# Optimization experiments

Hardware: AMD Instinct MI355X
Metric: run time of the kernel (lower is better)

The kernel has to match this reference:

```python
import jax, jax.numpy as jnp
import numpy as np

# FP4 E2M1 magnitude lookup table (3-bit magnitude index)
FP4_LUT = jnp.array([0.0, 0.5, 1.0, 1.5, 2.0, 3.0, 4.0, 6.0], dtype=jnp.float32)
E8M0_BIAS = 127


def setup_inputs() -> dict:
    key = jax.random.key(0)
    k_in, k_pw, k_sc, k_b = jax.random.split(key, 4)
    B, S, I, O, BS = 4, 2048, 4096, 11008, 32
    inp = jax.random.normal(k_in, (B, S, I), dtype=jnp.float32)
    # packed MXFP4 codes: two 4-bit codes per byte
    packed_weight = jax.random.randint(k_pw, (O, I // 2), 0, 256, dtype=jnp.int32)
    # E8M0 exponents near the bias so dequantized magnitudes are O(1)
    weight_scales = jax.random.randint(k_sc, (O, I // BS), 118, 132, dtype=jnp.int32)
    bias = jax.random.normal(k_b, (O,), dtype=jnp.float32) * 0.02
    return {"input": inp, "bias": bias, "packed_weight": packed_weight,
            "weight_scales": weight_scales}


def _dequantize_mxfp4(packed_weight, weight_scales):
    O, P = packed_weight.shape
    I = P * 2
    bs = I // weight_scales.shape[1]
    lo = packed_weight & 0xF          # first element of each pair: low nibble
    hi = (packed_weight >> 4) & 0xF   # second element: high nibble
    codes = jnp.stack([lo, hi], axis=-1).reshape(O, I)  # [O, I]
    mag = FP4_LUT[codes & 0x7]
    sign = jnp.where((codes & 0x8) > 0, -1.0, 1.0)
    vals = sign * mag                                   # [O, I] fp4 values
    scale = jnp.exp2((weight_scales - E8M0_BIAS).astype(jnp.float32))  # [O, I/bs]
    w = (vals.reshape(O, I // bs, bs) * scale[:, :, None]).reshape(O, I)
    return w


def reference(input, bias, packed_weight, weight_scales):
    # quantized-inference path: on-the-fly block dequant + F.linear
    w = _dequantize_mxfp4(packed_weight, weight_scales)  # [O, I]
    out = jnp.einsum('bsi,oi->bso', input, w) + bias     # [B, S, O]
    return out
```

## Files before the change

### kernel.cpp

```cpp
#include <hip/hip_runtime.h>
#include <stdint.h>

typedef __attribute__((ext_vector_type(8))) short bf16x8;
typedef __attribute__((ext_vector_type(8))) unsigned short u16x8;
typedef __attribute__((ext_vector_type(4))) float f32x4;
typedef __attribute__((ext_vector_type(4))) int i32x4;

static constexpr int MDIM = 8192;
static constexpr int KDIM = 4096;
static constexpr int NDIM = 11008;
static constexpr int BM = 256, BN = 256, BK = 32;
static constexpr int NT = KDIM / BK;
static constexpr int NBX = NDIM / BN;
static constexpr int NBY = MDIM / BM;


static __device__ __forceinline__ unsigned short f2bf(float f) {
  unsigned int u = __builtin_bit_cast(unsigned int, f);
  return (unsigned short)((u + 0x7FFFu + ((u >> 16) & 1u)) >> 16);
}

static __device__ __forceinline__ float fp4_val(unsigned int c) {
  unsigned int m = c & 1u, e = (c >> 1) & 3u, s = (c >> 3) & 1u;
  unsigned int bits = e ? (((126u + e) << 23) | (m << 22)) : (m ? 0x3F000000u : 0u);
  bits |= s << 31;
  return __builtin_bit_cast(float, bits);
}

__global__ __launch_bounds__(256) void convert_a_kernel(
    const float4* __restrict__ in, u16x8* __restrict__ out, int n8) {
  int i = blockIdx.x * 256 + threadIdx.x;
  if (i >= n8) return;
  float4 v0 = in[2 * (size_t)i];
  float4 v1 = in[2 * (size_t)i + 1];
  u16x8 r;
  r[0] = f2bf(v0.x); r[1] = f2bf(v0.y); r[2] = f2bf(v0.z); r[3] = f2bf(v0.w);
  r[4] = f2bf(v1.x); r[5] = f2bf(v1.y); r[6] = f2bf(v1.z); r[7] = f2bf(v1.w);
  out[i] = r;
}

__global__ __launch_bounds__(256) void dequant_w_kernel(
    const int* __restrict__ pw, const int* __restrict__ sc,
    unsigned short* __restrict__ wout) {
  int tid = blockIdx.x * 256 + threadIdx.x;
  int o = tid >> 7;
  int b = tid & 127;
  if (o >= NDIM) return;
  const i32x4* src = (const i32x4*)(pw + (size_t)o * (KDIM / 2) + b * 16);
  unsigned int e = (unsigned int)sc[(size_t)o * (KDIM / 32) + b];
  float scale = __builtin_bit_cast(float, e << 23);
  unsigned short* dst = wout + (size_t)o * KDIM + b * 32;
#pragma unroll
  for (int v = 0; v < 4; ++v) {
    i32x4 w4 = src[v];
    u16x8 r;
#pragma unroll
    for (int j = 0; j < 4; ++j) {
      unsigned int w = (unsigned int)w4[j];
      r[2 * j]     = f2bf(fp4_val(w & 0xFu) * scale);
      r[2 * j + 1] = f2bf(fp4_val((w >> 4) & 0xFu) * scale);
    }
    *(u16x8*)(dst + 8 * v) = r;
  }
}


#define GLDS16(gp, lp)                                                                  \
  __builtin_amdgcn_global_load_lds((const __attribute__((address_space(1))) void*)(gp), \
                                   (__attribute__((address_space(3))) void*)(lp), 16, 0, 0)

template <int CS, int NS, bool STAGE, bool LAST>
__device__ __forceinline__ void k_iter(
    unsigned char* lds, int p0, int p1,
    const unsigned short*& gA0, const unsigned short*& gA1,
    const unsigned short*& gB0, const unsigned short*& gB1,
    int baseA, int baseB, f32x4 (&acc)[8][4]) {
  if (LAST) asm volatile("s_waitcnt vmcnt(0)" ::: "memory");
  else      asm volatile("s_waitcnt vmcnt(4)" ::: "memory");
  __builtin_amdgcn_s_barrier();
  asm volatile("" ::: "memory");
  if (STAGE) {
    GLDS16(gA0, lds + NS * 32768 + p0);
    GLDS16(gA1, lds + NS * 32768 + p1);
    GLDS16(gB0, lds + NS * 32768 + 16384 + p0);
    GLDS16(gB1, lds + NS * 32768 + 16384 + p1);
    gA0 += BK; gA1 += BK; gB0 += BK; gB1 += BK;
  }
  const unsigned char* sa = lds + CS * 32768;
  const unsigned char* sb = sa + 16384;
  bf16x8 a[4], b[4];
#pragma unroll
  for (int m = 0; m < 4; ++m) a[m] = *(const bf16x8*)(sa + baseA + m * 1024);
#pragma unroll
  for (int n = 0; n < 4; ++n) b[n] = *(const bf16x8*)(sb + baseB + n * 1024);
  __builtin_amdgcn_s_setprio(1);
#pragma unroll
  for (int m = 0; m < 4; ++m)
#pragma unroll
    for (int n = 0; n < 4; ++n)
      acc[m][n] = __builtin_amdgcn_mfma_f32_16x16x32_bf16(a[m], b[n], acc[m][n], 0, 0, 0);
  __builtin_amdgcn_s_setprio(0);
  bf16x8 a2[4];
#pragma unroll
  for (int m = 0; m < 4; ++m) a2[m] = *(const bf16x8*)(sa + baseA + (4 + m) * 1024);
  __builtin_amdgcn_s_setprio(1);
#pragma unroll
  for (int m = 0; m < 4; ++m)
#pragma unroll
    for (int n = 0; n < 4; ++n)
      acc[4 + m][n] = __builtin_amdgcn_mfma_f32_16x16x32_bf16(a2[m], b[n], acc[4 + m][n], 0, 0, 0);
  __builtin_amdgcn_s_setprio(0);
}

__global__ __launch_bounds__(512, 2) void gemm_mx_kernel(
    const unsigned short* __restrict__ A,
    const unsigned short* __restrict__ Bw,
    const float* __restrict__ bias,
    float* __restrict__ C) {
  __shared__ __align__(16) unsigned char lds[3 * 32768];

  const int t = threadIdx.x;
  const int lane = t & 63;
  const int wave = t >> 6;
  const int wr = wave >> 2;
  const int wc = wave & 3;

  const int bid = blockIdx.x;
  const int swb = (bid & 7) * ((NBX * NBY) / 8) + (bid >> 3);
  const int by = swb / NBX;
  const int bx = swb - by * NBX;
  const int m0 = by * BM, n0 = bx * BN;

  const int fl = lane & 15;
  const int fh = lane >> 4;
  const int kof = (fh ^ ((fl >> 1) & 3)) * 16;
  const int baseA = (wr * 128 + fl) * 64 + kof;
  const int baseB = (wc * 64 + fl) * 64 + kof;

  const int p0 = t * 16, p1 = t * 16 + 8192;
  const int rA0 = p0 >> 6, rA1 = p1 >> 6;
  const int kb0 = ((((p0 >> 4) & 3) ^ ((p0 >> 7) & 3)) << 4);
  const int kb1 = ((((p1 >> 4) & 3) ^ ((p1 >> 7) & 3)) << 4);
  const unsigned short* gA0 = A + (size_t)(m0 + rA0) * KDIM + (kb0 >> 1);
  const unsigned short* gA1 = A + (size_t)(m0 + rA1) * KDIM + (kb1 >> 1);
  const unsigned short* gB0 = Bw + (size_t)(n0 + rA0) * KDIM + (kb0 >> 1);
  const unsigned short* gB1 = Bw + (size_t)(n0 + rA1) * KDIM + (kb1 >> 1);

  f32x4 acc[8][4] = {};

  GLDS16(gA0, lds + p0);
  GLDS16(gA1, lds + p1);
  GLDS16(gB0, lds + 16384 + p0);
  GLDS16(gB1, lds + 16384 + p1);
  gA0 += BK; gA1 += BK; gB0 += BK; gB1 += BK;
  GLDS16(gA0, lds + 32768 + p0);
  GLDS16(gA1, lds + 32768 + p1);
  GLDS16(gB0, lds + 32768 + 16384 + p0);
  GLDS16(gB1, lds + 32768 + 16384 + p1);
  gA0 += BK; gA1 += BK; gB0 += BK; gB1 += BK;

  for (int it = 0; it < 42; ++it) {
    k_iter<0, 2, true, false>(lds, p0, p1, gA0, gA1, gB0, gB1, baseA, baseB, acc);
    k_iter<1, 0, true, false>(lds, p0, p1, gA0, gA1, gB0, gB1, baseA, baseB, acc);
    k_iter<2, 1, true, false>(lds, p0, p1, gA0, gA1, gB0, gB1, baseA, baseB, acc);
  }
  k_iter<0, 2, false, false>(lds, p0, p1, gA0, gA1, gB0, gB1, baseA, baseB, acc);
  k_iter<1, 0, false, true>(lds, p0, p1, gA0, gA1, gB0, gB1, baseA, baseB, acc);

#pragma unroll
  for (int n = 0; n < 4; ++n) {
    const int gn = n0 + wc * 64 + n * 16 + fl;
    const float bv = bias[gn];
#pragma unroll
    for (int m = 0; m < 8; ++m) {
      const int gm = m0 + wr * 128 + m * 16 + fh * 4;
      float* cp = C + (size_t)gm * NDIM + gn;
#pragma unroll
      for (int r = 0; r < 4; ++r)
        cp[(size_t)r * NDIM] = acc[m][n][r] + bv;
    }
  }
}

extern "C" void kernel_launch(void* const* d_in, const int* in_sizes, int n_in,
                              void* d_out, int out_size, void* d_ws, size_t ws_size,
                              hipStream_t stream) {
  const float* inp  = (const float*)d_in[0];
  const float* bias = (const float*)d_in[1];
  const int* pw     = (const int*)d_in[2];
  const int* sc     = (const int*)d_in[3];
  float* out = (float*)d_out;

  unsigned short* a_bf = (unsigned short*)d_ws;
  unsigned short* w_bf = a_bf + (size_t)MDIM * KDIM;
  size_t need = ((size_t)MDIM * KDIM + (size_t)NDIM * KDIM) * sizeof(unsigned short);
  if (ws_size < need) return;

  {
    int n8 = MDIM * KDIM / 8;
    convert_a_kernel<<<dim3(n8 / 256), dim3(256), 0, stream>>>(
        (const float4*)inp, (u16x8*)a_bf, n8);
  }
  {
    int nthr = NDIM * (KDIM / 32);
    dequant_w_kernel<<<dim3(nthr / 256), dim3(256), 0, stream>>>(pw, sc, w_bf);
  }
  gemm_mx_kernel<<<dim3(NBX * NBY), dim3(512), 0, stream>>>(a_bf, w_bf, bias, out);
}
```

Before: 822.6 us.

## Double-buffer BK=64 GEMM with interleaved staged loads and merged prep kernel

Reworks the bf16 GEMM main loop from a triple-buffered BK=32 pipeline into a double-buffered BK=64 pipeline (64 KB per stage). Each tile is split into four MFMA phases with global-to-LDS loads for the next tile spread between them, and uses a new 8-way XOR swizzle for the 128-byte rows. The activation conversion and weight dequant kernels are also merged into one launch. The aim is fewer barriers per k step, better overlap of loads with MFMA, and one less kernel launch, at the cost of more LDS per block and more barriers inside each tile, which may limit occupancy to one block per CU.

```diff
diff --git a/kernel.cpp b/kernel.cpp
--- a/kernel.cpp
+++ b/kernel.cpp
@@ -9,8 +9,7 @@
 static constexpr int MDIM = 8192;
 static constexpr int KDIM = 4096;
 static constexpr int NDIM = 11008;
-static constexpr int BM = 256, BN = 256, BK = 32;
-static constexpr int NT = KDIM / BK;
+static constexpr int BM = 256, BN = 256, BK = 64;
 static constexpr int NBX = NDIM / BN;
 static constexpr int NBY = MDIM / BM;
 
@@ -27,40 +26,41 @@
   return __builtin_bit_cast(float, bits);
 }
 
-__global__ __launch_bounds__(256) void convert_a_kernel(
-    const float4* __restrict__ in, u16x8* __restrict__ out, int n8) {
-  int i = blockIdx.x * 256 + threadIdx.x;
-  if (i >= n8) return;
-  float4 v0 = in[2 * (size_t)i];
-  float4 v1 = in[2 * (size_t)i + 1];
-  u16x8 r;
-  r[0] = f2bf(v0.x); r[1] = f2bf(v0.y); r[2] = f2bf(v0.z); r[3] = f2bf(v0.w);
-  r[4] = f2bf(v1.x); r[5] = f2bf(v1.y); r[6] = f2bf(v1.z); r[7] = f2bf(v1.w);
-  out[i] = r;
-}
-
-__global__ __launch_bounds__(256) void dequant_w_kernel(
+static constexpr int CONV_BLOCKS = (MDIM * KDIM / 8) / 256;
+static constexpr int DEQ_BLOCKS  = (NDIM * (KDIM / 32)) / 256;
+
+__global__ __launch_bounds__(256) void prep_kernel(
+    const float4* __restrict__ in, u16x8* __restrict__ aout,
     const int* __restrict__ pw, const int* __restrict__ sc,
     unsigned short* __restrict__ wout) {
-  int tid = blockIdx.x * 256 + threadIdx.x;
-  int o = tid >> 7;
-  int b = tid & 127;
-  if (o >= NDIM) return;
-  const i32x4* src = (const i32x4*)(pw + (size_t)o * (KDIM / 2) + b * 16);
-  unsigned int e = (unsigned int)sc[(size_t)o * (KDIM / 32) + b];
-  float scale = __builtin_bit_cast(float, e << 23);
-  unsigned short* dst = wout + (size_t)o * KDIM + b * 32;
-#pragma unroll
-  for (int v = 0; v < 4; ++v) {
-    i32x4 w4 = src[v];
+  if (blockIdx.x < CONV_BLOCKS) {
+    int i = blockIdx.x * 256 + threadIdx.x;
+    float4 v0 = in[2 * (size_t)i];
+    float4 v1 = in[2 * (size_t)i + 1];
     u16x8 r;
-#pragma unroll
-    for (int j = 0; j < 4; ++j) {
-      unsigned int w = (unsigned int)w4[j];
-      r[2 * j]     = f2bf(fp4_val(w & 0xFu) * scale);
-      r[2 * j + 1] = f2bf(fp4_val((w >> 4) & 0xFu) * scale);
+    r[0] = f2bf(v0.x); r[1] = f2bf(v0.y); r[2] = f2bf(v0.z); r[3] = f2bf(v0.w);
+    r[4] = f2bf(v1.x); r[5] = f2bf(v1.y); r[6] = f2bf(v1.z); r[7] = f2bf(v1.w);
+    aout[i] = r;
+  } else {
+    int tid = (blockIdx.x - CONV_BLOCKS) * 256 + threadIdx.x;
+    int o = tid >> 7;
+    int b = tid & 127;
+    const i32x4* src = (const i32x4*)(pw + (size_t)o * (KDIM / 2) + b * 16);
+    unsigned int e = (unsigned int)sc[(size_t)o * (KDIM / 32) + b];
+    float scale = __builtin_bit_cast(float, e << 23);
+    unsigned short* dst = wout + (size_t)o * KDIM + b * 32;
+#pragma unroll
+    for (int v = 0; v < 4; ++v) {
+      i32x4 w4 = src[v];
+      u16x8 r;
+#pragma unroll
+      for (int j = 0; j < 4; ++j) {
+        unsigned int w = (unsigned int)w4[j];
+        r[2 * j]     = f2bf(fp4_val(w & 0xFu) * scale);
+        r[2 * j + 1] = f2bf(fp4_val((w >> 4) & 0xFu) * scale);
+      }
+      *(u16x8*)(dst + 8 * v) = r;
     }
-    *(u16x8*)(dst + 8 * v) = r;
   }
 }
 
@@ -69,47 +69,80 @@
   __builtin_amdgcn_global_load_lds((const __attribute__((address_space(1))) void*)(gp), \
                                    (__attribute__((address_space(3))) void*)(lp), 16, 0, 0)
 
-template <int CS, int NS, bool STAGE, bool LAST>
-__device__ __forceinline__ void k_iter(
-    unsigned char* lds, int p0, int p1,
-    const unsigned short*& gA0, const unsigned short*& gA1,
-    const unsigned short*& gB0, const unsigned short*& gB1,
-    int baseA, int baseB, f32x4 (&acc)[8][4]) {
-  if (LAST) asm volatile("s_waitcnt vmcnt(0)" ::: "memory");
-  else      asm volatile("s_waitcnt vmcnt(4)" ::: "memory");
-  __builtin_amdgcn_s_barrier();
-  asm volatile("" ::: "memory");
-  if (STAGE) {
-    GLDS16(gA0, lds + NS * 32768 + p0);
-    GLDS16(gA1, lds + NS * 32768 + p1);
-    GLDS16(gB0, lds + NS * 32768 + 16384 + p0);
-    GLDS16(gB1, lds + NS * 32768 + 16384 + p1);
-    gA0 += BK; gA1 += BK; gB0 += BK; gB1 += BK;
-  }
-  const unsigned char* sa = lds + CS * 32768;
-  const unsigned char* sb = sa + 16384;
-  bf16x8 a[4], b[4];
-#pragma unroll
-  for (int m = 0; m < 4; ++m) a[m] = *(const bf16x8*)(sa + baseA + m * 1024);
-#pragma unroll
-  for (int n = 0; n < 4; ++n) b[n] = *(const bf16x8*)(sb + baseB + n * 1024);
-  __builtin_amdgcn_s_setprio(1);
-#pragma unroll
-  for (int m = 0; m < 4; ++m)
-#pragma unroll
-    for (int n = 0; n < 4; ++n)
-      acc[m][n] = __builtin_amdgcn_mfma_f32_16x16x32_bf16(a[m], b[n], acc[m][n], 0, 0, 0);
-  __builtin_amdgcn_s_setprio(0);
-  bf16x8 a2[4];
-#pragma unroll
-  for (int m = 0; m < 4; ++m) a2[m] = *(const bf16x8*)(sa + baseA + (4 + m) * 1024);
-  __builtin_amdgcn_s_setprio(1);
-#pragma unroll
-  for (int m = 0; m < 4; ++m)
-#pragma unroll
-    for (int n = 0; n < 4; ++n)
-      acc[4 + m][n] = __builtin_amdgcn_mfma_f32_16x16x32_bf16(a2[m], b[n], acc[4 + m][n], 0, 0, 0);
-  __builtin_amdgcn_s_setprio(0);
+#define BAR() asm volatile("s_barrier" ::: "memory")
+
+#define MFMA16(ACC, AV, BV, MO)                                                          \
+  _Pragma("unroll") for (int m_ = 0; m_ < 4; ++m_)                                       \
+  _Pragma("unroll") for (int n_ = 0; n_ < 4; ++n_)                                       \
+      ACC[MO + m_][n_] = __builtin_amdgcn_mfma_f32_16x16x32_bf16(AV[m_], BV[n_],         \
+                                                                 ACC[MO + m_][n_], 0, 0, 0)
+
+template <int SLOT, bool STAGE>
+__device__ __forceinline__ void ktile(
+    unsigned char* lds, const unsigned short*& gA, const unsigned short*& gB,
+    int stq, int aBase, int bBase, int kof0, int kof1, f32x4 (&acc)[8][4]) {
+  const unsigned char* sa = lds + SLOT * 65536;
+  const unsigned char* sb = sa + 32768;
+  unsigned char* da = lds + (SLOT ^ 1) * 65536 + stq;
+  unsigned char* db = da + 32768;
+  bf16x8 a[4], b[4], a2[4];
+
+#pragma unroll
+  for (int m = 0; m < 4; ++m) a[m] = *(const bf16x8*)(sa + aBase + m * 2048 + kof0);
+#pragma unroll
+  for (int n = 0; n < 4; ++n) b[n] = *(const bf16x8*)(sb + bBase + n * 2048 + kof0);
+  if (STAGE) {
+    GLDS16(gB, db);
+    GLDS16(gB + (size_t)64 * KDIM, db + 8192);
+    asm volatile("s_waitcnt vmcnt(2)" ::: "memory");
+  } else {
+    asm volatile("s_waitcnt vmcnt(0)" ::: "memory");
+  }
+  BAR();
+  __builtin_amdgcn_s_setprio(1);
+  MFMA16(acc, a, b, 0);
+  __builtin_amdgcn_s_setprio(0);
+  BAR();
+
+#pragma unroll
+  for (int m = 0; m < 4; ++m) a2[m] = *(const bf16x8*)(sa + aBase + (4 + m) * 2048 + kof0);
+  if (STAGE) {
+    GLDS16(gB + (size_t)128 * KDIM, db + 16384);
+    GLDS16(gB + (size_t)192 * KDIM, db + 24576);
+  }
+  BAR();
+  __builtin_amdgcn_s_setprio(1);
+  MFMA16(acc, a2, b, 4);
+  __builtin_amdgcn_s_setprio(0);
+  BAR();
+
+#pragma unroll
+  for (int m = 0; m < 4; ++m) a[m] = *(const bf16x8*)(sa + aBase + m * 2048 + kof1);
+#pragma unroll
+  for (int n = 0; n < 4; ++n) b[n] = *(const bf16x8*)(sb + bBase + n * 2048 + kof1);
+  if (STAGE) {
+    GLDS16(gA, da);
+    GLDS16(gA + (size_t)128 * KDIM, da + 16384);
+  }
+  BAR();
+  __builtin_amdgcn_s_setprio(1);
+  MFMA16(acc, a, b, 0);
+  __builtin_amdgcn_s_setprio(0);
+  BAR();
+
+#pragma unroll
+  for (int m = 0; m < 4; ++m) a2[m] = *(const bf16x8*)(sa + aBase + (4 + m) * 2048 + kof1);
+  if (STAGE) {
+    GLDS16(gA + (size_t)64 * KDIM, da + 8192);
+    GLDS16(gA + (size_t)192 * KDIM, da + 24576);
+    gA += BK; gB += BK;
+    asm volatile("s_waitcnt vmcnt(2)" ::: "memory");
+  }
+  BAR();
+  __builtin_amdgcn_s_setprio(1);
+  MFMA16(acc, a2, b, 4);
+  __builtin_amdgcn_s_setprio(0);
+  BAR();
 }
 
 __global__ __launch_bounds__(512, 2) void gemm_mx_kernel(
@@ -117,7 +150,7 @@
     const unsigned short* __restrict__ Bw,
     const float* __restrict__ bias,
     float* __restrict__ C) {
-  __shared__ __align__(16) unsigned char lds[3 * 32768];
+  __shared__ __align__(16) unsigned char lds[2 * 65536];
 
   const int t = threadIdx.x;
   const int lane = t & 63;
@@ -133,39 +166,41 @@
 
   const int fl = lane & 15;
   const int fh = lane >> 4;
-  const int kof = (fh ^ ((fl >> 1) & 3)) * 16;
-  const int baseA = (wr * 128 + fl) * 64 + kof;
-  const int baseB = (wc * 64 + fl) * 64 + kof;
-
-  const int p0 = t * 16, p1 = t * 16 + 8192;
-  const int rA0 = p0 >> 6, rA1 = p1 >> 6;
-  const int kb0 = ((((p0 >> 4) & 3) ^ ((p0 >> 7) & 3)) << 4);
-  const int kb1 = ((((p1 >> 4) & 3) ^ ((p1 >> 7) & 3)) << 4);
-  const unsigned short* gA0 = A + (size_t)(m0 + rA0) * KDIM + (kb0 >> 1);
-  const unsigned short* gA1 = A + (size_t)(m0 + rA1) * KDIM + (kb1 >> 1);
-  const unsigned short* gB0 = Bw + (size_t)(n0 + rA0) * KDIM + (kb0 >> 1);
-  const unsigned short* gB1 = Bw + (size_t)(n0 + rA1) * KDIM + (kb1 >> 1);
+  const int kof0 = ((fh)     ^ (fl & 7)) * 16;
+  const int kof1 = ((4 + fh) ^ (fl & 7)) * 16;
+  const int aBase = (wr * 128 + fl) * 128;
+  const int bBase = (wc * 64 + fl) * 128;
+
+  const int stq = t * 16;
+  const int srow = t >> 3;
+  const int koff = 8 * ((t & 7) ^ (srow & 7));
+  const unsigned short* gA = A + (size_t)(m0 + srow) * KDIM + koff;
+  const unsigned short* gB = Bw + (size_t)(n0 + srow) * KDIM + koff;
 
   f32x4 acc[8][4] = {};
 
-  GLDS16(gA0, lds + p0);
-  GLDS16(gA1, lds + p1);
-  GLDS16(gB0, lds + 16384 + p0);
-  GLDS16(gB1, lds + 16384 + p1);
-  gA0 += BK; gA1 += BK; gB0 += BK; gB1 += BK;
-  GLDS16(gA0, lds + 32768 + p0);
-  GLDS16(gA1, lds + 32768 + p1);
-  GLDS16(gB0, lds + 32768 + 16384 + p0);
-  GLDS16(gB1, lds + 32768 + 16384 + p1);
-  gA0 += BK; gA1 += BK; gB0 += BK; gB1 += BK;
-
-  for (int it = 0; it < 42; ++it) {
-    k_iter<0, 2, true, false>(lds, p0, p1, gA0, gA1, gB0, gB1, baseA, baseB, acc);
-    k_iter<1, 0, true, false>(lds, p0, p1, gA0, gA1, gB0, gB1, baseA, baseB, acc);
-    k_iter<2, 1, true, false>(lds, p0, p1, gA0, gA1, gB0, gB1, baseA, baseB, acc);
-  }
-  k_iter<0, 2, false, false>(lds, p0, p1, gA0, gA1, gB0, gB1, baseA, baseB, acc);
-  k_iter<1, 0, false, true>(lds, p0, p1, gA0, gA1, gB0, gB1, baseA, baseB, acc);
+  {
+    unsigned char* da = lds + stq;
+    unsigned char* db = da + 32768;
+    GLDS16(gB, db);
+    GLDS16(gB + (size_t)64 * KDIM, db + 8192);
+    GLDS16(gB + (size_t)128 * KDIM, db + 16384);
+    GLDS16(gB + (size_t)192 * KDIM, db + 24576);
+    GLDS16(gA, da);
+    GLDS16(gA + (size_t)128 * KDIM, da + 16384);
+    GLDS16(gA + (size_t)64 * KDIM, da + 8192);
+    GLDS16(gA + (size_t)192 * KDIM, da + 24576);
+    gA += BK; gB += BK;
+    asm volatile("s_waitcnt vmcnt(2)" ::: "memory");
+    BAR();
+  }
+
+  for (int it = 0; it < 31; ++it) {
+    ktile<0, true>(lds, gA, gB, stq, aBase, bBase, kof0, kof1, acc);
+    ktile<1, true>(lds, gA, gB, stq, aBase, bBase, kof0, kof1, acc);
+  }
+  ktile<0, true>(lds, gA, gB, stq, aBase, bBase, kof0, kof1, acc);
+  ktile<1, false>(lds, gA, gB, stq, aBase, bBase, kof0, kof1, acc);
 
 #pragma unroll
   for (int n = 0; n < 4; ++n) {
@@ -196,14 +231,7 @@
   size_t need = ((size_t)MDIM * KDIM + (size_t)NDIM * KDIM) * sizeof(unsigned short);
   if (ws_size < need) return;
 
-  {
-    int n8 = MDIM * KDIM / 8;
-    convert_a_kernel<<<dim3(n8 / 256), dim3(256), 0, stream>>>(
-        (const float4*)inp, (u16x8*)a_bf, n8);
-  }
-  {
-    int nthr = NDIM * (KDIM / 32);
-    dequant_w_kernel<<<dim3(nthr / 256), dim3(256), 0, stream>>>(pw, sc, w_bf);
-  }
+  prep_kernel<<<dim3(CONV_BLOCKS + DEQ_BLOCKS), dim3(256), 0, stream>>>(
+      (const float4*)inp, (u16x8*)a_bf, pw, sc, w_bf);
   gemm_mx_kernel<<<dim3(NBX * NBY), dim3(512), 0, stream>>>(a_bf, w_bf, bias, out);
 }
```

After: 859.7 us. +4.5%, slower.
